# Performance work log

Hardware: AMD Instinct MI355X
Metric: run time of the kernel (lower is better)

The kernel has to match this reference:

```python
import jax, jax.numpy as jnp
import numpy as np

DIM = 256
H = 4
K = 16
R = 4
EPS = 1e-5


def _conv1x1(x, W, b):
    # x: [B, Cin, N, P], W: [Cout, Cin], b: [Cout]
    return jnp.einsum('oc,bcnp->bonp', W, x) + b[None, :, None, None]


def setup_inputs() -> dict:
    key = jax.random.key(0)
    ks = jax.random.split(key, 12)
    B, N = 4, 8192
    s = 1.0 / np.sqrt(DIM)
    inp = {
        'queries': jax.random.normal(ks[0], (B, DIM, N, R), dtype=jnp.float32),
        'feats': jax.random.normal(ks[1], (B, DIM, N, K), dtype=jnp.float32),
        'Wq': jax.random.normal(ks[2], (DIM, DIM), dtype=jnp.float32) * s,
        'bq': jnp.zeros((DIM,), dtype=jnp.float32),
        'Wk': jax.random.normal(ks[3], (DIM, DIM), dtype=jnp.float32) * s,
        'bk': jnp.zeros((DIM,), dtype=jnp.float32),
        'Wv': jax.random.normal(ks[4], (DIM, DIM), dtype=jnp.float32) * s,
        'bv': jnp.zeros((DIM,), dtype=jnp.float32),
        'W1': jax.random.normal(ks[5], (2 * DIM, DIM), dtype=jnp.float32) * s,
        'b1': jnp.zeros((2 * DIM,), dtype=jnp.float32),
        'gamma': jnp.ones((2 * DIM,), dtype=jnp.float32),
        'beta': jnp.zeros((2 * DIM,), dtype=jnp.float32),
        'W2': jax.random.normal(ks[6], (DIM, 2 * DIM), dtype=jnp.float32) * (1.0 / np.sqrt(2 * DIM)),
        'b2': jnp.zeros((DIM,), dtype=jnp.float32),
    }
    return inp


def reference(queries, feats, Wq, bq, Wk, bk, Wv, bv, W1, b1, gamma, beta, W2, b2):
    B, _, N, _ = feats.shape
    d = DIM // H
    queries_iden = queries  # [B, dim, N, r]

    q = _conv1x1(queries, Wq, bq).reshape(B, H, d, N, R)   # [B,h,d,N,r]
    k = _conv1x1(feats, Wk, bk).reshape(B, H, d, N, K)     # [B,h,d,N,K]
    v = _conv1x1(feats, Wv, bv).reshape(B, H, d, N, K)     # [B,h,d,N,K]

    # logits: [B,N,h,r,K]
    logits = jnp.einsum('bhdnr,bhdnk->bnhrk', q, k) * (d ** -0.5)
    soft = jax.nn.softmax(logits, axis=-1)
    # agg: [B,N,h,r,d] -> permute to [B,N,h,d,r] -> [B,N,dim,r] -> [B,dim,N,r]
    agg = jnp.einsum('bnhrk,bhdnk->bnhdr', soft, v)
    agg = agg.reshape(B, N, DIM, R).transpose(0, 2, 1, 3)
    agg = agg + queries_iden

    # FFN: conv1x1 -> BN (training-mode batch stats) -> ReLU -> conv1x1, residual, ReLU
    h1 = _conv1x1(agg, W1, b1)  # [B, 2*dim, N, r]
    mean = jnp.mean(h1, axis=(0, 2, 3), keepdims=True)
    var = jnp.var(h1, axis=(0, 2, 3), keepdims=True)
    h1 = (h1 - mean) * jax.lax.rsqrt(var + EPS)
    h1 = h1 * gamma[None, :, None, None] + beta[None, :, None, None]
    h1 = jax.nn.relu(h1)
    h2 = _conv1x1(h1, W2, b2)
    return jax.nn.relu(h2 + agg)
```

## Files before the change

### kernel.cpp

```cpp
#include <hip/hip_runtime.h>
#include <hip/hip_bf16.h>

#define NB 4
#define NRQ 32768
#define NKF 131072

using u16 = unsigned short;
typedef short bf16x8 __attribute__((ext_vector_type(8)));
typedef float f32x4  __attribute__((ext_vector_type(4)));
typedef u16   u16x8  __attribute__((ext_vector_type(8)));
typedef u16   u16x4  __attribute__((ext_vector_type(4)));
typedef u16   u16x2  __attribute__((ext_vector_type(2)));

#if defined(__has_builtin)
#  if __has_builtin(__builtin_amdgcn_fdot2_f32_bf16)
#    define HAVE_DOT2 1
#  endif
#endif
#ifndef HAVE_DOT2
#  define HAVE_DOT2 0
#endif

#if HAVE_DOT2
typedef __bf16 bfv2 __attribute__((ext_vector_type(2)));
union bpack { bf16x8 v; bfv2 p[4]; };
__device__ __forceinline__ float dot2(bfv2 a, bfv2 b, float c){
  return __builtin_amdgcn_fdot2_f32_bf16(a, b, c, false);
}
#endif
union vpack { bf16x8 v; u16 e[8]; };

__device__ __forceinline__ u16 f2b(float f){
  __hip_bfloat16 h = __float2bfloat16(f);
  return *reinterpret_cast<u16*>(&h);
}
__device__ __forceinline__ float b2f(u16 v){
  return __uint_as_float(((unsigned)v) << 16);
}

#define GLOAD16(g, l) __builtin_amdgcn_global_load_lds( \
    (const __attribute__((address_space(1))) unsigned int*)(g), \
    (__attribute__((address_space(3))) unsigned int*)(l), 16, 0, 0)

__global__ __launch_bounds__(256) void cvtW_k(
    const float* __restrict__ Wk, const float* __restrict__ Wv,
    const float* __restrict__ Wq, const float* __restrict__ W1,
    const float* __restrict__ W2, u16* __restrict__ wT,
    const float* __restrict__ bk, const float* __restrict__ bv,
    float* __restrict__ bKV, float* __restrict__ stats)
{
  if (blockIdx.x >= 224){
    int i = (blockIdx.x - 224) * 256 + threadIdx.x;
    if (i < 512)       bKV[i] = (i < 256) ? bk[i] : bv[i - 256];
    else if (i < 1536) stats[i - 512] = 0.f;
    return;
  }
  long e = ((long)blockIdx.x * 256 + threadIdx.x) * 8;
  const float* src; long off;
  if      (e < 65536)  { src = Wk; off = e; }
  else if (e < 131072) { src = Wv; off = e - 65536; }
  else if (e < 196608) { src = Wq; off = e - 131072; }
  else if (e < 327680) { src = W1; off = e - 196608; }
  else                 { src = W2; off = e - 327680; }
  float4 f0 = *reinterpret_cast<const float4*>(src + off);
  float4 f1 = *reinterpret_cast<const float4*>(src + off + 4);
  u16x8 p;
  p[0]=f2b(f0.x); p[1]=f2b(f0.y); p[2]=f2b(f0.z); p[3]=f2b(f0.w);
  p[4]=f2b(f1.x); p[5]=f2b(f1.y); p[6]=f2b(f1.z); p[7]=f2b(f1.w);
  *reinterpret_cast<u16x8*>(wT + e) = p;
}

__global__ __launch_bounds__(256) void transpose_k(
    const float* __restrict__ in, u16* __restrict__ out,
    int NCtot, long outBatch)
{
  __shared__ u16 sT[64][264];
  const int t = threadIdx.x, b = blockIdx.y;
  const int nr0 = blockIdx.x * 64;
  const int cb = t >> 2, nrq = t & 3;
  const long ib = (long)b * 256 * NCtot + nr0;

  #pragma unroll
  for (int ci = 0; ci < 4; ++ci){
    const int c = cb + ci * 64;
    const float* src = in + ib + (long)c * NCtot + nrq * 16;
    #pragma unroll
    for (int j = 0; j < 4; ++j){
      float4 f = *reinterpret_cast<const float4*>(src + j * 4);
      int nr = nrq * 16 + j * 4;
      sT[nr+0][c] = f2b(f.x); sT[nr+1][c] = f2b(f.y);
      sT[nr+2][c] = f2b(f.z); sT[nr+3][c] = f2b(f.w);
    }
  }
  __syncthreads();
  const int row = t >> 2, qtr = t & 3;
  u16* orow = out + (long)b * outBatch + (long)(nr0 + row) * 256 + qtr * 64;
  #pragma unroll
  for (int i = 0; i < 8; ++i)
    *reinterpret_cast<u16x8*>(orow + i * 8) =
        *reinterpret_cast<const u16x8*>(&sT[row][qtr * 64 + i * 8]);
}

template<int MODE, int KD>
__global__ __launch_bounds__(256) void gemm_k(
    const u16* __restrict__ A, long aBatch, int chTiles,
    const u16* __restrict__ Wb, const float* __restrict__ bias,
    u16* __restrict__ outH, long oBatch, int NCH,
    float* __restrict__ statSum, float* __restrict__ statSq,
    const float* __restrict__ xsc, const float* __restrict__ xsh,
    const u16* __restrict__ residT,
    float* __restrict__ outF, long fBatch)
{
  __shared__ __align__(16) char sA[2][16384];
  __shared__ __align__(16) char sB[2][16384];

  const int t = threadIdx.x, lane = t & 63, wid = t >> 6;
  const int wm = wid >> 1, wn = wid & 1;
  const int b = blockIdx.z;

  const int nwg = gridDim.x, orig = blockIdx.x;
  const int qq = nwg >> 3, rr = nwg & 7, xcd = orig & 7, pos = orig >> 3;
  const int wg = (xcd < rr ? xcd * (qq + 1) : rr * (qq + 1) + (xcd - rr) * qq) + pos;
  const int rowT = wg / chTiles, chT = wg % chTiles;

  const u16* Ab = A + (long)b * aBatch + (long)rowT * 128 * KD;
  const u16* Wt = Wb + (long)chT * 128 * KD;
  const int sub = lane >> 3, kc8 = ((lane & 7) ^ sub) * 8;

  f32x4 acc[4][4];
  #pragma unroll
  for (int i = 0; i < 4; ++i)
    #pragma unroll
    for (int j = 0; j < 4; ++j) acc[i][j] = (f32x4){0.f,0.f,0.f,0.f};

  auto STAGE = [&](int buf, int ks){
    const int k0 = ks * 64;
    if constexpr (MODE == 3){
      const int wrow = t >> 1, whalf = t & 1;
      const u16* arow = Ab + (long)wrow * KD + k0 + whalf * 32;
      #pragma unroll
      for (int i = 0; i < 4; ++i){
        u16x8 v = *reinterpret_cast<const u16x8*>(arow + i * 8);
        const int kb = k0 + whalf*32 + i*8;
        float4 s0 = *reinterpret_cast<const float4*>(xsc + kb);
        float4 s1 = *reinterpret_cast<const float4*>(xsc + kb + 4);
        float4 h0 = *reinterpret_cast<const float4*>(xsh + kb);
        float4 h1 = *reinterpret_cast<const float4*>(xsh + kb + 4);
        u16x8 o;
        o[0]=f2b(fmaxf(b2f(v[0])*s0.x+h0.x,0.f));
        o[1]=f2b(fmaxf(b2f(v[1])*s0.y+h0.y,0.f));
        o[2]=f2b(fmaxf(b2f(v[2])*s0.z+h0.z,0.f));
        o[3]=f2b(fmaxf(b2f(v[3])*s0.w+h0.w,0.f));
        o[4]=f2b(fmaxf(b2f(v[4])*s1.x+h1.x,0.f));
        o[5]=f2b(fmaxf(b2f(v[5])*s1.y+h1.y,0.f));
        o[6]=f2b(fmaxf(b2f(v[6])*s1.z+h1.z,0.f));
        o[7]=f2b(fmaxf(b2f(v[7])*s1.w+h1.w,0.f));
        *reinterpret_cast<u16x8*>(
            sA[buf] + ((wrow*128 + whalf*64 + i*16) ^ ((wrow & 7) << 4))) = o;
      }
      #pragma unroll
      for (int i = 0; i < 4; ++i){
        const int chunk = wid * 4 + i;
        GLOAD16(Wt + (long)(chunk*8 + sub)*KD + k0 + kc8, sB[buf] + chunk*1024);
      }
    } else {
      #pragma unroll
      for (int i = 0; i < 4; ++i){
        const int chunk = wid * 4 + i;
        GLOAD16(Ab + (long)(chunk*8 + sub)*KD + k0 + kc8, sA[buf] + chunk*1024);
        GLOAD16(Wt + (long)(chunk*8 + sub)*KD + k0 + kc8, sB[buf] + chunk*1024);
      }
    }
  };

  constexpr int NT = KD / 64;
  STAGE(0, 0);
  __syncthreads();
  int cur = 0;
  for (int ks = 0; ks < NT; ++ks){
    if (ks + 1 < NT) STAGE(cur ^ 1, ks + 1);
    const char* pA = sA[cur]; const char* pB = sB[cur];
    #pragma unroll
    for (int kk = 0; kk < 2; ++kk){
      bf16x8 af[4], bf[4];
      #pragma unroll
      for (int mi = 0; mi < 4; ++mi){
        int m = wm*64 + mi*16 + (lane & 15);
        af[mi] = *reinterpret_cast<const bf16x8*>(
            pA + ((m*128 + kk*64 + (lane>>4)*16) ^ ((m & 7) << 4)));
      }
      #pragma unroll
      for (int ni = 0; ni < 4; ++ni){
        int c = wn*64 + ni*16 + (lane & 15);
        bf[ni] = *reinterpret_cast<const bf16x8*>(
            pB + ((c*128 + kk*64 + (lane>>4)*16) ^ ((c & 7) << 4)));
      }
      #pragma unroll
      for (int mi = 0; mi < 4; ++mi)
        #pragma unroll
        for (int ni = 0; ni < 4; ++ni)
          acc[mi][ni] = __builtin_amdgcn_mfma_f32_16x16x32_bf16(
              af[mi], bf[ni], acc[mi][ni], 0, 0, 0);
    }
    __syncthreads();
    cur ^= 1;
  }

  int chI[4]; float bv[4];
  #pragma unroll
  for (int ni = 0; ni < 4; ++ni){
    int ch = chT*128 + wn*64 + ni*16 + (lane & 15);
    chI[ni] = ch;
    bv[ni] = bias[ch];
  }
  if (MODE != 3){
    float s[4] = {0,0,0,0}, sq[4] = {0,0,0,0};
    u16* outb = outH + (long)b * oBatch;
    #pragma unroll
    for (int mi = 0; mi < 4; ++mi){
      #pragma unroll
      for (int j = 0; j < 4; ++j){
        const long row = rowT*128 + wm*64 + mi*16 + (lane>>4)*4 + j;
        #pragma unroll
        for (int ni = 0; ni < 4; ++ni){
          float v = acc[mi][ni][j] + bv[ni];
          outb[row * NCH + chI[ni]] = f2b(v);
          if (MODE == 1){ s[ni] += v; sq[ni] += v * v; }
        }
      }
    }
    if (MODE == 1){
      #pragma unroll
      for (int ni = 0; ni < 4; ++ni){
        s[ni]  += __shfl_xor(s[ni], 16);  s[ni]  += __shfl_xor(s[ni], 32);
        sq[ni] += __shfl_xor(sq[ni], 16); sq[ni] += __shfl_xor(sq[ni], 32);
      }
      if (lane < 16){
        #pragma unroll
        for (int ni = 0; ni < 4; ++ni){
          atomicAdd(&statSum[chI[ni]], s[ni]);
          atomicAdd(&statSq[chI[ni]],  sq[ni]);
        }
      }
    }
  } else {
    const u16* rb = residT + (long)b * ((long)NRQ * 256);
    #pragma unroll
    for (int mi = 0; mi < 4; ++mi){
      const int nr0 = rowT*128 + wm*64 + mi*16 + (lane>>4)*4;
      #pragma unroll
      for (int ni = 0; ni < 4; ++ni){
        float4 o;
        o.x = fmaxf(acc[mi][ni][0] + bv[ni] + b2f(rb[(long)(nr0+0)*256 + chI[ni]]), 0.f);
        o.y = fmaxf(acc[mi][ni][1] + bv[ni] + b2f(rb[(long)(nr0+1)*256 + chI[ni]]), 0.f);
        o.z = fmaxf(acc[mi][ni][2] + bv[ni] + b2f(rb[(long)(nr0+2)*256 + chI[ni]]), 0.f);
        o.w = fmaxf(acc[mi][ni][3] + bv[ni] + b2f(rb[(long)(nr0+3)*256 + chI[ni]]), 0.f);
        *reinterpret_cast<float4*>(outF + (long)b*fBatch + (long)chI[ni]*NRQ + nr0) = o;
      }
    }
  }
}

__global__ __launch_bounds__(1024, 1) void kvattn_k(
    const float* __restrict__ feats, const u16* __restrict__ wKV,
    const float* __restrict__ bKV, const u16* __restrict__ qT,
    const u16* __restrict__ qrT, u16* __restrict__ aggT)
{
  __shared__ __align__(16) char LDS[142848];
  char*  sAg = LDS;
  char*  sW  = LDS + 18432;
  char*  sK  = LDS;
  char*  sV  = LDS + 67584;
  float* sSf = (float*)(LDS + 134144);

  const int t = threadIdx.x, lane = t & 63, wid = t >> 6;
  const int wr = wid >> 2, wc = wid & 3;
  const int b = blockIdx.y;
  const long row0 = (long)blockIdx.x * 128;

  const int chL = t >> 5, nq = t & 31;
  const float* fbase = feats + (long)b * 256 * NKF + row0 + nq * 4;

  auto STAGEW = [&](int buf, int ks){
    const int k0 = ks * 32;
    #pragma unroll
    for (int i = 0; i < 2; ++i){
      const int cw = wid * 2 + i;
      const int ch = cw * 16 + (lane >> 2), jd = lane & 3;
      GLOAD16(wKV + (long)ch * 256 + k0 + ((jd ^ ((ch >> 1) & 3)) * 8),
              sW + buf * 32768 + cw * 1024);
    }
  };
  auto WRITEA = [&](int buf, float4 f){
    #pragma unroll
    for (int i = 0; i < 4; ++i){
      const int r = nq * 4 + i;
      float e = (i == 0) ? f.x : (i == 1) ? f.y : (i == 2) ? f.z : f.w;
      *reinterpret_cast<u16*>(sAg + buf*9216 + r*72 + chL*2) = f2b(e);
    }
  };

  f32x4 acc[2][8];
  #pragma unroll
  for (int i = 0; i < 2; ++i)
    #pragma unroll
    for (int j = 0; j < 8; ++j) acc[i][j] = (f32x4){0.f,0.f,0.f,0.f};

  float4 aReg0, aReg1;
  {
    aReg0 = *reinterpret_cast<const float4*>(fbase + (long)chL * NKF);
    aReg1 = *reinterpret_cast<const float4*>(fbase + (long)(32 + chL) * NKF);
    STAGEW(0, 0);
    WRITEA(0, aReg0);
  }
  __syncthreads();

  int cur = 0;
  const int jq = lane >> 4;
  #pragma unroll
  for (int ks = 0; ks < 8; ++ks){
    if (ks < 7) STAGEW(cur ^ 1, ks + 1);
    __builtin_amdgcn_sched_barrier(0);
    if (ks < 6){
      float4 f = *reinterpret_cast<const float4*>(
          fbase + (long)((ks + 2) * 32 + chL) * NKF);
      if ((ks & 1) == 0) aReg0 = f; else aReg1 = f;
    }
    const char* pA = sAg + cur * 9216;
    const char* pW = sW  + cur * 32768;
    bf16x8 af[2];
    #pragma unroll
    for (int mi = 0; mi < 2; ++mi){
      const int m = wr*32 + mi*16 + (lane & 15);
      af[mi] = *reinterpret_cast<const bf16x8*>(pA + m*72 + jq*16);
    }
    __builtin_amdgcn_s_setprio(1);
    #pragma unroll
    for (int ni = 0; ni < 8; ++ni){
      const int ch = wc*128 + ni*16 + (lane & 15);
      bf16x8 bf = *reinterpret_cast<const bf16x8*>(
          pW + ch*64 + (((jq ^ ((ch>>1)&3)) * 16)));
      acc[0][ni] = __builtin_amdgcn_mfma_f32_16x16x32_bf16(af[0], bf, acc[0][ni], 0,0,0);
      acc[1][ni] = __builtin_amdgcn_mfma_f32_16x16x32_bf16(af[1], bf, acc[1][ni], 0,0,0);
    }
    __builtin_amdgcn_s_setprio(0);
    if (ks < 7) WRITEA(cur ^ 1, ((ks + 1) & 1) == 0 ? aReg0 : aReg1);
    if (ks < 6){
      asm volatile("s_waitcnt vmcnt(1) lgkmcnt(0)" ::: "memory");
    } else {
      asm volatile("s_waitcnt vmcnt(0) lgkmcnt(0)" ::: "memory");
    }
    __builtin_amdgcn_s_barrier();
    cur ^= 1;
  }

  {
    float bv[8];
    #pragma unroll
    for (int ni = 0; ni < 8; ++ni) bv[ni] = bKV[wc*128 + ni*16 + (lane & 15)];
    if (wc < 2){
      #pragma unroll
      for (int mi = 0; mi < 2; ++mi){
        #pragma unroll
        for (int ni = 0; ni < 8; ++ni){
          const int ch = wc*128 + ni*16 + (lane & 15);
          #pragma unroll
          for (int j = 0; j < 4; ++j){
            const int r = wr*32 + mi*16 + (lane>>4)*4 + j;
            *reinterpret_cast<u16*>(sK + r*528 + ch*2) =
                f2b(acc[mi][ni][j] + bv[ni]);
          }
        }
      }
    } else {
      #pragma unroll
      for (int mi = 0; mi < 2; ++mi){
        #pragma unroll
        for (int ni = 0; ni < 8; ++ni){
          const int cv = (wc-2)*128 + ni*16 + (lane & 15);
          #pragma unroll
          for (int j = 0; j < 4; ++j){
            const int r = wr*32 + mi*16 + (lane>>4)*4 + j;
            *reinterpret_cast<u16*>(sV + r*520 + cv*2) =
                f2b(acc[mi][ni][j] + bv[ni]);
          }
        }
      }
    }
  }

  const int p = wid >> 1, rh = wid & 1;
  const int nqg = blockIdx.x * 8 + p;
  const int c0 = rh*128 + lane*2;
  u16x2 rq[4];
  {
    const u16* rqp = qrT + ((long)b*NRQ + (long)nqg*4)*256 + c0;
    #pragma unroll
    for (int r = 0; r < 4; ++r)
      rq[r] = *reinterpret_cast<const u16x2*>(rqp + r*256);
  }
  __syncthreads();

  {
    const int h = lane >> 4, kk = lane & 15;
    const u16* qb = qT + ((long)b*NRQ + (long)nqg*4 + rh*2)*256 + h*64;
    const char* kr = sK + (p*16 + kk)*528 + h*128;
    float l0 = 0.f, l1 = 0.f;
#if HAVE_DOT2
    #pragma unroll
    for (int d8 = 0; d8 < 8; ++d8){
      bpack K8, Q0, Q1;
      K8.v = *reinterpret_cast<const bf16x8*>(kr + d8*16);
      Q0.v = *reinterpret_cast<const bf16x8*>(qb + d8*8);
      Q1.v = *reinterpret_cast<const bf16x8*>(qb + 256 + d8*8);
      #pragma unroll
      for (int pi = 0; pi < 4; ++pi){
        l0 = dot2(K8.p[pi], Q0.p[pi], l0);
        l1 = dot2(K8.p[pi], Q1.p[pi], l1);
      }
    }
#else
    #pragma unroll
    for (int d8 = 0; d8 < 8; ++d8){
      vpack K8, Q0, Q1;
      K8.v = *reinterpret_cast<const bf16x8*>(kr + d8*16);
      Q0.v = *reinterpret_cast<const bf16x8*>(qb + d8*8);
      Q1.v = *reinterpret_cast<const bf16x8*>(qb + 256 + d8*8);
      #pragma unroll
      for (int e = 0; e < 8; ++e){
        float kf = b2f(K8.e[e]);
        l0 = fmaf(kf, b2f(Q0.e[e]), l0);
        l1 = fmaf(kf, b2f(Q1.e[e]), l1);
      }
    }
#endif
    float pr[2]; float lv[2] = {l0, l1};
    #pragma unroll
    for (int r = 0; r < 2; ++r){
      float x = lv[r] * 0.125f;
      float m = x;
      #pragma unroll
      for (int off = 1; off < 16; off <<= 1) m = fmaxf(m, __shfl_xor(m, off));
      float e = __expf(x - m);
      float ssum = e;
      #pragma unroll
      for (int off = 1; off < 16; off <<= 1) ssum += __shfl_xor(ssum, off);
      pr[r] = e / ssum;
    }
    *reinterpret_cast<float2*>(sSf + (p*4 + h)*68 + kk*4 + rh*2) =
        make_float2(pr[0], pr[1]);
  }
  __syncthreads();

  {
    const int h = c0 >> 6;
    const char* vrow = sV + (p*16)*520;
    const float* ss = sSf + (p*4 + h)*68;
    float a[4][2] = {};
    #pragma unroll
    for (int kk = 0; kk < 16; ++kk){
      u16x2 vv = *reinterpret_cast<const u16x2*>(vrow + kk*520 + c0*2);
      float4 sv = *reinterpret_cast<const float4*>(ss + kk*4);
      float v0 = b2f(vv[0]), v1 = b2f(vv[1]);
      a[0][0] += sv.x*v0; a[0][1] += sv.x*v1;
      a[1][0] += sv.y*v0; a[1][1] += sv.y*v1;
      a[2][0] += sv.z*v0; a[2][1] += sv.z*v1;
      a[3][0] += sv.w*v0; a[3][1] += sv.w*v1;
    }
    u16* ob = aggT + ((long)b*NRQ + (long)nqg*4)*256 + c0;
    #pragma unroll
    for (int r = 0; r < 4; ++r){
      u16x2 pk;
      pk[0] = f2b(a[r][0] + b2f(rq[r][0]));
      pk[1] = f2b(a[r][1] + b2f(rq[r][1]));
      *reinterpret_cast<u16x2*>(ob + r*256) = pk;
    }
  }
}

__global__ void finalize_k(const float* __restrict__ st,
                           const float* __restrict__ gamma,
                           const float* __restrict__ beta,
                           float* __restrict__ out)
{
  int o = blockIdx.x*256 + threadIdx.x;
  const float inv = 1.f / 131072.f;
  float mean = st[o] * inv;
  float var  = st[512 + o] * inv - mean*mean;
  float sc   = gamma[o] * rsqrtf(var + 1e-5f);
  out[o]       = sc;
  out[512 + o] = beta[o] - mean * sc;
}

extern "C" void kernel_launch(void* const* d_in, const int* in_sizes, int n_in,
                              void* d_out, int out_size, void* d_ws, size_t ws_size,
                              hipStream_t stream)
{
  (void)in_sizes; (void)n_in; (void)out_size; (void)ws_size;
  const float* queries = (const float*)d_in[0];
  const float* feats   = (const float*)d_in[1];
  const float* Wq = (const float*)d_in[2];
  const float* bq = (const float*)d_in[3];
  const float* Wk = (const float*)d_in[4];
  const float* bk = (const float*)d_in[5];
  const float* Wv = (const float*)d_in[6];
  const float* bv = (const float*)d_in[7];
  const float* W1 = (const float*)d_in[8];
  const float* b1 = (const float*)d_in[9];
  const float* gamma = (const float*)d_in[10];
  const float* beta  = (const float*)d_in[11];
  const float* W2 = (const float*)d_in[12];
  const float* b2 = (const float*)d_in[13];

  char* ws = (char*)d_ws;
  u16*   h1T   = (u16*)ws;
  u16*   qrT   = (u16*)(ws + 134217728L);
  u16*   qT    = (u16*)(ws + 201326592L);
  u16*   aggT  = (u16*)(ws + 268435456L);
  float* stats = (float*)(ws + 335544320L);
  float* scale = stats + 1024;
  float* shift = stats + 1536;
  u16*   wT    = (u16*)(ws + 335552512L);
  u16*   wKV   = wT;
  u16*   wQ    = wT + 131072;
  u16*   wW1   = wT + 196608;
  u16*   wW2   = wT + 327680;
  float* bKV   = (float*)(wT + 458752);

  cvtW_k<<<dim3(230), 256, 0, stream>>>(Wk, Wv, Wq, W1, W2, wT,
                                        bk, bv, bKV, stats);

  transpose_k<<<dim3(NRQ/64, NB), 256, 0, stream>>>(queries, qrT, NRQ, (long)NRQ*256);

  gemm_k<0, 256><<<dim3(512, 1, NB), 256, 0, stream>>>(
      qrT, (long)NRQ*256, 2, wQ, bq,
      qT, (long)NRQ*256, 256, nullptr, nullptr, nullptr, nullptr,
      nullptr, nullptr, 0);

  kvattn_k<<<dim3(NKF/128, NB), 1024, 0, stream>>>(
      feats, wKV, bKV, qT, qrT, aggT);

  gemm_k<1, 256><<<dim3(1024, 1, NB), 256, 0, stream>>>(
      aggT, (long)NRQ*256, 4, wW1, b1,
      h1T, (long)NRQ*512, 512, stats, stats + 512, nullptr, nullptr,
      nullptr, nullptr, 0);

  finalize_k<<<dim3(2), 256, 0, stream>>>(stats, gamma, beta, scale);

  gemm_k<3, 512><<<dim3(512, 1, NB), 256, 0, stream>>>(
      h1T, (long)NRQ*512, 2, wW2, b2,
      nullptr, 0, 256, nullptr, nullptr, scale, shift,
      aggT, (float*)d_out, (long)256*NRQ);
}
```

Measured before the change: 667.3 us.

## Halve kvattn block size to 512 threads with doubled per-wave work

Reworks the fused K/V projection and attention kernel to use 512 threads per block, with each wave computing four MFMA row tiles instead of two. Each wave now handles all four query rows per point, with wider vector loads in the softmax and aggregation stages. Feature loads become scalar strided loads, and the hand-tuned waitcnt/barrier pipeline is replaced by a plain __syncthreads. LDS use is still ~140KB per block, so the launch_bounds(512,2) hint probably cannot give two blocks per CU. The change also risks higher register pressure and less load/compute overlap.

```diff
diff --git a/kernel.cpp b/kernel.cpp
--- a/kernel.cpp
+++ b/kernel.cpp
@@ -23,12 +23,14 @@
 
 #if HAVE_DOT2
 typedef __bf16 bfv2 __attribute__((ext_vector_type(2)));
-union bpack { bf16x8 v; bfv2 p[4]; };
+union bpack  { bf16x8 v; bfv2 p[4]; };
+union bpack4 { u16x4  v; bfv2 p[2]; };
 __device__ __forceinline__ float dot2(bfv2 a, bfv2 b, float c){
   return __builtin_amdgcn_fdot2_f32_bf16(a, b, c, false);
 }
 #endif
-union vpack { bf16x8 v; u16 e[8]; };
+union vpack  { bf16x8 v; u16 e[8]; };
+union vpack4 { u16x4 v; u16 e[4]; };
 
 __device__ __forceinline__ u16 f2b(float f){
   __hip_bfloat16 h = __float2bfloat16(f);
@@ -261,7 +263,7 @@
   }
 }
 
-__global__ __launch_bounds__(1024, 1) void kvattn_k(
+__global__ __launch_bounds__(512, 2) void kvattn_k(
     const float* __restrict__ feats, const u16* __restrict__ wKV,
     const float* __restrict__ bKV, const u16* __restrict__ qT,
     const u16* __restrict__ qrT, u16* __restrict__ aggT)
@@ -278,40 +280,43 @@
   const int b = blockIdx.y;
   const long row0 = (long)blockIdx.x * 128;
 
-  const int chL = t >> 5, nq = t & 31;
-  const float* fbase = feats + (long)b * 256 * NKF + row0 + nq * 4;
+  const int chL = t >> 4, nq = t & 15;
+  const float* fbase = feats + (long)b * 256 * NKF + row0 + nq;
 
   auto STAGEW = [&](int buf, int ks){
     const int k0 = ks * 32;
     #pragma unroll
-    for (int i = 0; i < 2; ++i){
-      const int cw = wid * 2 + i;
+    for (int i = 0; i < 4; ++i){
+      const int cw = wid * 4 + i;
       const int ch = cw * 16 + (lane >> 2), jd = lane & 3;
       GLOAD16(wKV + (long)ch * 256 + k0 + ((jd ^ ((ch >> 1) & 3)) * 8),
               sW + buf * 32768 + cw * 1024);
     }
   };
-  auto WRITEA = [&](int buf, float4 f){
-    #pragma unroll
-    for (int i = 0; i < 4; ++i){
-      const int r = nq * 4 + i;
-      float e = (i == 0) ? f.x : (i == 1) ? f.y : (i == 2) ? f.z : f.w;
-      *reinterpret_cast<u16*>(sAg + buf*9216 + r*72 + chL*2) = f2b(e);
-    }
+  auto LOADA = [&](int ks, float* ar){
+    const float* src = fbase + (long)(ks * 32 + chL) * NKF;
+    #pragma unroll
+    for (int i = 0; i < 8; ++i) ar[i] = src[16 * i];
   };
-
-  f32x4 acc[2][8];
+  auto WRITEA = [&](int buf, const float* ar){
+    #pragma unroll
+    for (int i = 0; i < 8; ++i){
+      const int r = nq + 16 * i;
+      *reinterpret_cast<u16*>(sAg + buf*9216 + r*72 + chL*2) = f2b(ar[i]);
+    }
+  };
+
+  f32x4 acc[4][8];
   #pragma unroll
-  for (int i = 0; i < 2; ++i)
+  for (int i = 0; i < 4; ++i)
     #pragma unroll
     for (int j = 0; j < 8; ++j) acc[i][j] = (f32x4){0.f,0.f,0.f,0.f};
 
-  float4 aReg0, aReg1;
+  float aR[8];
   {
-    aReg0 = *reinterpret_cast<const float4*>(fbase + (long)chL * NKF);
-    aReg1 = *reinterpret_cast<const float4*>(fbase + (long)(32 + chL) * NKF);
+    LOADA(0, aR);
     STAGEW(0, 0);
-    WRITEA(0, aReg0);
+    WRITEA(0, aR);
   }
   __syncthreads();
 
@@ -319,19 +324,16 @@
   const int jq = lane >> 4;
   #pragma unroll
   for (int ks = 0; ks < 8; ++ks){
-    if (ks < 7) STAGEW(cur ^ 1, ks + 1);
-    __builtin_amdgcn_sched_barrier(0);
-    if (ks < 6){
-      float4 f = *reinterpret_cast<const float4*>(
-          fbase + (long)((ks + 2) * 32 + chL) * NKF);
-      if ((ks & 1) == 0) aReg0 = f; else aReg1 = f;
+    if (ks < 7){
+      LOADA(ks + 1, aR);
+      STAGEW(cur ^ 1, ks + 1);
     }
     const char* pA = sAg + cur * 9216;
     const char* pW = sW  + cur * 32768;
-    bf16x8 af[2];
-    #pragma unroll
-    for (int mi = 0; mi < 2; ++mi){
-      const int m = wr*32 + mi*16 + (lane & 15);
+    bf16x8 af[4];
+    #pragma unroll
+    for (int mi = 0; mi < 4; ++mi){
+      const int m = wr*64 + mi*16 + (lane & 15);
       af[mi] = *reinterpret_cast<const bf16x8*>(pA + m*72 + jq*16);
     }
     __builtin_amdgcn_s_setprio(1);
@@ -340,17 +342,14 @@
       const int ch = wc*128 + ni*16 + (lane & 15);
       bf16x8 bf = *reinterpret_cast<const bf16x8*>(
           pW + ch*64 + (((jq ^ ((ch>>1)&3)) * 16)));
-      acc[0][ni] = __builtin_amdgcn_mfma_f32_16x16x32_bf16(af[0], bf, acc[0][ni], 0,0,0);
-      acc[1][ni] = __builtin_amdgcn_mfma_f32_16x16x32_bf16(af[1], bf, acc[1][ni], 0,0,0);
+      #pragma unroll
+      for (int mi = 0; mi < 4; ++mi)
+        acc[mi][ni] = __builtin_amdgcn_mfma_f32_16x16x32_bf16(
+            af[mi], bf, acc[mi][ni], 0, 0, 0);
     }
     __builtin_amdgcn_s_setprio(0);
-    if (ks < 7) WRITEA(cur ^ 1, ((ks + 1) & 1) == 0 ? aReg0 : aReg1);
-    if (ks < 6){
-      asm volatile("s_waitcnt vmcnt(1) lgkmcnt(0)" ::: "memory");
-    } else {
-      asm volatile("s_waitcnt vmcnt(0) lgkmcnt(0)" ::: "memory");
-    }
-    __builtin_amdgcn_s_barrier();
+    if (ks < 7) WRITEA(cur ^ 1, aR);
+    __syncthreads();
     cur ^= 1;
   }
 
@@ -358,86 +357,72 @@
     float bv[8];
     #pragma unroll
     for (int ni = 0; ni < 8; ++ni) bv[ni] = bKV[wc*128 + ni*16 + (lane & 15)];
-    if (wc < 2){
-      #pragma unroll
-      for (int mi = 0; mi < 2; ++mi){
+    char* dst = (wc < 2) ? sK : sV;
+    const int pitch = (wc < 2) ? 528 : 520;
+    const int chb = (wc & 1) * 128;
+    #pragma unroll
+    for (int mi = 0; mi < 4; ++mi){
+      #pragma unroll
+      for (int ni = 0; ni < 8; ++ni){
+        const int ch = chb + ni*16 + (lane & 15);
         #pragma unroll
-        for (int ni = 0; ni < 8; ++ni){
-          const int ch = wc*128 + ni*16 + (lane & 15);
-          #pragma unroll
-          for (int j = 0; j < 4; ++j){
-            const int r = wr*32 + mi*16 + (lane>>4)*4 + j;
-            *reinterpret_cast<u16*>(sK + r*528 + ch*2) =
-                f2b(acc[mi][ni][j] + bv[ni]);
-          }
+        for (int j = 0; j < 4; ++j){
+          const int r = wr*64 + mi*16 + (lane>>4)*4 + j;
+          *reinterpret_cast<u16*>(dst + r*pitch + ch*2) =
+              f2b(acc[mi][ni][j] + bv[ni]);
         }
       }
-    } else {
-      #pragma unroll
-      for (int mi = 0; mi < 2; ++mi){
-        #pragma unroll
-        for (int ni = 0; ni < 8; ++ni){
-          const int cv = (wc-2)*128 + ni*16 + (lane & 15);
-          #pragma unroll
-          for (int j = 0; j < 4; ++j){
-            const int r = wr*32 + mi*16 + (lane>>4)*4 + j;
-            *reinterpret_cast<u16*>(sV + r*520 + cv*2) =
-                f2b(acc[mi][ni][j] + bv[ni]);
-          }
-        }
-      }
-    }
-  }
-
-  const int p = wid >> 1, rh = wid & 1;
+    }
+  }
+
+  const int p = wid;
   const int nqg = blockIdx.x * 8 + p;
-  const int c0 = rh*128 + lane*2;
-  u16x2 rq[4];
+  const int c0 = lane * 4;
+  u16x4 rq[4];
   {
     const u16* rqp = qrT + ((long)b*NRQ + (long)nqg*4)*256 + c0;
     #pragma unroll
     for (int r = 0; r < 4; ++r)
-      rq[r] = *reinterpret_cast<const u16x2*>(rqp + r*256);
+      rq[r] = *reinterpret_cast<const u16x4*>(rqp + r*256);
   }
   __syncthreads();
 
   {
     const int h = lane >> 4, kk = lane & 15;
-    const u16* qb = qT + ((long)b*NRQ + (long)nqg*4 + rh*2)*256 + h*64;
+    const u16* qb = qT + ((long)b*NRQ + (long)nqg*4)*256 + h*64;
     const char* kr = sK + (p*16 + kk)*528 + h*128;
-    float l0 = 0.f, l1 = 0.f;
+    float l[4] = {0.f, 0.f, 0.f, 0.f};
 #if HAVE_DOT2
     #pragma unroll
     for (int d8 = 0; d8 < 8; ++d8){
-      bpack K8, Q0, Q1;
+      bpack K8;
       K8.v = *reinterpret_cast<const bf16x8*>(kr + d8*16);
-      Q0.v = *reinterpret_cast<const bf16x8*>(qb + d8*8);
-      Q1.v = *reinterpret_cast<const bf16x8*>(qb + 256 + d8*8);
-      #pragma unroll
-      for (int pi = 0; pi < 4; ++pi){
-        l0 = dot2(K8.p[pi], Q0.p[pi], l0);
-        l1 = dot2(K8.p[pi], Q1.p[pi], l1);
+      #pragma unroll
+      for (int r = 0; r < 4; ++r){
+        bpack Q;
+        Q.v = *reinterpret_cast<const bf16x8*>(qb + r*256 + d8*8);
+        #pragma unroll
+        for (int pi = 0; pi < 4; ++pi) l[r] = dot2(K8.p[pi], Q.p[pi], l[r]);
       }
     }
 #else
     #pragma unroll
     for (int d8 = 0; d8 < 8; ++d8){
-      vpack K8, Q0, Q1;
+      vpack K8;
       K8.v = *reinterpret_cast<const bf16x8*>(kr + d8*16);
-      Q0.v = *reinterpret_cast<const bf16x8*>(qb + d8*8);
-      Q1.v = *reinterpret_cast<const bf16x8*>(qb + 256 + d8*8);
-      #pragma unroll
-      for (int e = 0; e < 8; ++e){
-        float kf = b2f(K8.e[e]);
-        l0 = fmaf(kf, b2f(Q0.e[e]), l0);
-        l1 = fmaf(kf, b2f(Q1.e[e]), l1);
+      #pragma unroll
+      for (int r = 0; r < 4; ++r){
+        vpack Q;
+        Q.v = *reinterpret_cast<const bf16x8*>(qb + r*256 + d8*8);
+        #pragma unroll
+        for (int e = 0; e < 8; ++e) l[r] = fmaf(b2f(K8.e[e]), b2f(Q.e[e]), l[r]);
       }
     }
 #endif
-    float pr[2]; float lv[2] = {l0, l1};
-    #pragma unroll
-    for (int r = 0; r < 2; ++r){
-      float x = lv[r] * 0.125f;
+    float4 prob;
+    #pragma unroll
+    for (int r = 0; r < 4; ++r){
+      float x = l[r] * 0.125f;
       float m = x;
       #pragma unroll
       for (int off = 1; off < 16; off <<= 1) m = fmaxf(m, __shfl_xor(m, off));
@@ -445,10 +430,11 @@
       float ssum = e;
       #pragma unroll
       for (int off = 1; off < 16; off <<= 1) ssum += __shfl_xor(ssum, off);
-      pr[r] = e / ssum;
-    }
-    *reinterpret_cast<float2*>(sSf + (p*4 + h)*68 + kk*4 + rh*2) =
-        make_float2(pr[0], pr[1]);
+      float pr = e / ssum;
+      if (r == 0) prob.x = pr; else if (r == 1) prob.y = pr;
+      else if (r == 2) prob.z = pr; else prob.w = pr;
+    }
+    *reinterpret_cast<float4*>(sSf + (p*4 + h)*68 + kk*4) = prob;
   }
   __syncthreads();
 
@@ -456,24 +442,26 @@
     const int h = c0 >> 6;
     const char* vrow = sV + (p*16)*520;
     const float* ss = sSf + (p*4 + h)*68;
-    float a[4][2] = {};
+    float a[4][4] = {};
     #pragma unroll
     for (int kk = 0; kk < 16; ++kk){
-      u16x2 vv = *reinterpret_cast<const u16x2*>(vrow + kk*520 + c0*2);
+      vpack4 vv;
+      vv.v = *reinterpret_cast<const u16x4*>(vrow + kk*520 + c0*2);
       float4 sv = *reinterpret_cast<const float4*>(ss + kk*4);
-      float v0 = b2f(vv[0]), v1 = b2f(vv[1]);
-      a[0][0] += sv.x*v0; a[0][1] += sv.x*v1;
-      a[1][0] += sv.y*v0; a[1][1] += sv.y*v1;
-      a[2][0] += sv.z*v0; a[2][1] += sv.z*v1;
-      a[3][0] += sv.w*v0; a[3][1] += sv.w*v1;
+      #pragma unroll
+      for (int cc = 0; cc < 4; ++cc){
+        float vf = b2f(vv.e[cc]);
+        a[0][cc] += sv.x*vf; a[1][cc] += sv.y*vf;
+        a[2][cc] += sv.z*vf; a[3][cc] += sv.w*vf;
+      }
     }
     u16* ob = aggT + ((long)b*NRQ + (long)nqg*4)*256 + c0;
     #pragma unroll
     for (int r = 0; r < 4; ++r){
-      u16x2 pk;
-      pk[0] = f2b(a[r][0] + b2f(rq[r][0]));
-      pk[1] = f2b(a[r][1] + b2f(rq[r][1]));
-      *reinterpret_cast<u16x2*>(ob + r*256) = pk;
+      u16x4 pk;
+      #pragma unroll
+      for (int cc = 0; cc < 4; ++cc) pk[cc] = f2b(a[r][cc] + b2f(rq[r][cc]));
+      *reinterpret_cast<u16x4*>(ob + r*256) = pk;
     }
   }
 }
@@ -537,7 +525,7 @@
       qT, (long)NRQ*256, 256, nullptr, nullptr, nullptr, nullptr,
       nullptr, nullptr, 0);
 
-  kvattn_k<<<dim3(NKF/128, NB), 1024, 0, stream>>>(
+  kvattn_k<<<dim3(NKF/128, NB), 512, 0, stream>>>(
       feats, wKV, bKV, qT, qrT, aggT);
 
   gemm_k<1, 256><<<dim3(1024, 1, NB), 256, 0, stream>>>(
```

Result: no change. 657.8 us (-1.4%).
